# Optimization experiments

Measured on AMD Instinct MI355X. Metric: run time of the kernel, lower is better.

## Reference

```python
import jax, jax.numpy as jnp
import numpy as np

NEG_SLOPE = 0.01  # nn.LeakyReLU default


def setup_inputs() -> dict:
    key = jax.random.key(0)
    ks = jax.random.split(key, 13)
    B, T, C = 128, 2048, 16
    CO = 8 * C          # 128 conv out channels == LSTM input
    H = 128             # LSTM hidden
    G = 4 * H           # gate dim
    OUT = 1
    s = 0.08            # keep recurrence stable over 2048 steps
    f32 = jnp.float32
    return {
        "x": jax.random.normal(ks[0], (B, T, C), f32),
        "conv_w": jax.random.normal(ks[1], (CO, C, 3), f32) * s,
        "conv_b": jax.random.normal(ks[2], (CO,), f32) * s,
        "w_ih0": jax.random.normal(ks[3], (G, CO), f32) * s,
        "w_hh0": jax.random.normal(ks[4], (G, H), f32) * s,
        "b_ih0": jax.random.normal(ks[5], (G,), f32) * s,
        "b_hh0": jax.random.normal(ks[6], (G,), f32) * s,
        "w_ih1": jax.random.normal(ks[7], (G, H), f32) * s,
        "w_hh1": jax.random.normal(ks[8], (G, H), f32) * s,
        "b_ih1": jax.random.normal(ks[9], (G,), f32) * s,
        "b_hh1": jax.random.normal(ks[10], (G,), f32) * s,
        "lin_w": jax.random.normal(ks[11], (OUT, H), f32) * s,
        "lin_b": jax.random.normal(ks[12], (OUT,), f32) * s,
    }


def _lstm_cell(gates, c):
    i, f, g, o = jnp.split(gates, 4, axis=-1)  # torch gate order i,f,g,o
    c_new = jax.nn.sigmoid(f) * c + jax.nn.sigmoid(i) * jnp.tanh(g)
    h_new = jax.nn.sigmoid(o) * jnp.tanh(c_new)
    return h_new, c_new


def reference(x, conv_w, conv_b, w_ih0, w_hh0, b_ih0, b_hh0,
              w_ih1, w_hh1, b_ih1, b_hh1, lin_w, lin_b):
    B, T, C = x.shape
    H = w_hh0.shape[1]
    # Conv1d k=3 pad=1 over time: [B,C,T] -> [B,8C,T]
    xc = jnp.transpose(x, (0, 2, 1))
    y = jax.lax.conv_general_dilated(
        xc, conv_w, window_strides=(1,), padding=((1, 1),),
        dimension_numbers=("NCH", "OIH", "NCH"))
    y = y + conv_b[None, :, None]
    y = jnp.where(y >= 0, y, NEG_SLOPE * y)  # LeakyReLU
    seq = jnp.transpose(y, (0, 2, 1))  # [B,T,8C]
    # Precompute layer-0 input projection (biases folded in, constant per step)
    x0 = jnp.einsum("btc,gc->btg", seq, w_ih0) + (b_ih0 + b_hh0)  # [B,T,4H]
    b1 = b_ih1 + b_hh1

    def step(carry, xt):
        h0, c0, h1, c1 = carry
        h0, c0 = _lstm_cell(xt + h0 @ w_hh0.T, c0)
        h1, c1 = _lstm_cell(h0 @ w_ih1.T + b1 + h1 @ w_hh1.T, c1)
        return (h0, c0, h1, c1), h1

    zeros = jnp.zeros((B, H), x.dtype)
    init = (zeros, zeros, zeros, zeros)
    xs = jnp.transpose(x0, (1, 0, 2))  # [T,B,4H]
    _, hs = jax.lax.scan(step, init, xs)  # [T,B,H]
    pooled = hs.mean(axis=0)  # adaptive_avg_pool1d(.,1) == mean over time
    return pooled @ lin_w.T + lin_b
```

## Files before the change

kernel.cpp:

```cpp
#include <hip/hip_runtime.h>
#include <hip/hip_fp16.h>
#include <cstdint>
#include <cstddef>

#define B_ 128
#define T_ 2048
#define C_ 16
#define CO_ 128
#define H_ 128
#define G_ 512
#define WCV 184
#define NBLK (72 + WCV)
#define L2E  1.4426950408889634f
#define L2E2 2.8853900817779268f

typedef _Float16 half8 __attribute__((ext_vector_type(8)));
typedef float f32x4 __attribute__((ext_vector_type(4)));

__device__ __forceinline__ unsigned packh2f(float a, float b) {
  union { _Float16 h[2]; unsigned u; } x;
  x.h[0] = (_Float16)a; x.h[1] = (_Float16)b;
  return x.u;
}

__device__ __forceinline__ float rcpf(float x) { return __builtin_amdgcn_rcpf(x); }

__device__ __forceinline__ float exp2f_(float x) {
#if __has_builtin(__builtin_amdgcn_exp2f)
  return __builtin_amdgcn_exp2f(x);
#else
  return __expf(x * 0.6931471805599453f);
#endif
}

__device__ __forceinline__ void block_sync() {
  asm volatile("s_waitcnt lgkmcnt(0)" ::: "memory");
  __builtin_amdgcn_s_barrier();
  asm volatile("" ::: "memory");
}

__device__ __forceinline__ int ld_rlx(const int* p) {
  return __hip_atomic_load(p, __ATOMIC_RELAXED, __HIP_MEMORY_SCOPE_AGENT);
}
__device__ __forceinline__ void st_rlx(int* p, int v) {
  __hip_atomic_store(p, v, __ATOMIC_RELAXED, __HIP_MEMORY_SCOPE_AGENT);
}

__device__ __forceinline__ float lstm_cell1(float iv, float fv, float gv,
                                            float ov, float& c) {
  gv = fminf(fmaxf(gv, -43.3f), 43.3f);
  float ei = exp2f_(-iv), ef = exp2f_(-fv), eg = exp2f_(gv);
  float P = (1.f + ei) * (eg + 1.f);
  float Q = 1.f + ef;
  float num = c * P + (eg - 1.f) * Q;
  float cN = num * rcpf(Q * P);
  c = cN;
  float cc = fminf(fmaxf(cN, -15.f), 15.f);
  float eo = exp2f_(-ov), ec = exp2f_(L2E2 * cc);
  return (ec - 1.f) * rcpf((1.f + eo) * (ec + 1.f));
}

__global__ __launch_bounds__(256) void pack_kernel(
    const float* __restrict__ w_ih0, const float* __restrict__ w_hh0,
    const float* __restrict__ w_ih1, const float* __restrict__ w_hh1,
    const float* __restrict__ b_ih1, const float* __restrict__ b_hh1,
    uint4* __restrict__ Wf0, uint4* __restrict__ Wih1f,
    uint4* __restrict__ Whh1f, uint4* __restrict__ WB0f,
    f32x4* __restrict__ b1fD) {
  int tid = blockIdx.x * 256 + threadIdx.x;
  if (tid < 24576) {
    int u = tid & 8191, L = u & 63, s = (u >> 6) & 3, tl = (u >> 8) & 3, w = u >> 10;
    int which = tid >> 13;
    const float* src = (which == 0) ? w_hh0 : (which == 1) ? w_ih1 : w_hh1;
    uint4* dst = (which == 0) ? Wf0 : (which == 1) ? Wih1f : Whh1f;
    int m = (w + 8 * tl) * 16 + (L & 15);
    float sc = (tl == 2) ? L2E2 : L2E;
    int k0 = s * 32 + (L >> 4) * 8;
    const float* p = src + m * 128 + k0;
    uint4 o;
    o.x = packh2f(p[0] * sc, p[1] * sc); o.y = packh2f(p[2] * sc, p[3] * sc);
    o.z = packh2f(p[4] * sc, p[5] * sc); o.w = packh2f(p[6] * sc, p[7] * sc);
    dst[u] = o;
  } else if (tid < 32768) {
    int u = tid - 24576, L = u & 63, s = (u >> 6) & 3, nt = u >> 8;
    int g = nt * 16 + (L & 15);
    float sc = ((nt >> 3) == 2) ? L2E2 : L2E;
    int k0 = s * 32 + (L >> 4) * 8;
    const float* p = w_ih0 + g * 128 + k0;
    uint4 o;
    o.x = packh2f(p[0] * sc, p[1] * sc); o.y = packh2f(p[2] * sc, p[3] * sc);
    o.z = packh2f(p[4] * sc, p[5] * sc); o.w = packh2f(p[6] * sc, p[7] * sc);
    WB0f[u] = o;
  } else if (tid < 34816) {
    int u2 = tid - 32768;
    int tl = u2 & 3, L = (u2 >> 2) & 63, w = u2 >> 8;
    int q = L >> 4;
    float sc = (tl == 2) ? L2E2 : L2E;
    f32x4 o;
#pragma unroll
    for (int reg = 0; reg < 4; ++reg) {
      int row = (w + 8 * tl) * 16 + q * 4 + reg;
      o[reg] = (b_ih1[row] + b_hh1[row]) * sc;
    }
    b1fD[u2] = o;
  }
}

__global__ __launch_bounds__(512, 1) void persist_kernel(
    const float* __restrict__ x, const float* __restrict__ conv_w,
    const float* __restrict__ conv_b, const float* __restrict__ b_ih0,
    const float* __restrict__ b_hh0,
    const uint4* __restrict__ Wf0, const uint4* __restrict__ Wih1f,
    const uint4* __restrict__ Whh1f, const uint4* __restrict__ WB0f,
    const f32x4* __restrict__ b1fD,
    uint4* __restrict__ x0f, uint2* __restrict__ h0g, uint4* __restrict__ z1f,
    float* __restrict__ psave, int* __restrict__ flags,
    int rmask, int rmask2) {
  __shared__ __align__(16) union {
    struct { float xs[34 * 16]; _Float16 yh[32 * 136]; _Float16 x0S[32 * 512]; } wk;
    struct { _Float16 h[2][16 * 136]; float red[8192]; } rc;
  } sm;

  int* xready = flags;
  int* l0p = flags + 2048;
  int* l0c = flags + 2560;
  int* z1p = flags + 3072;
  int* l1p = flags + 3200;

  const int bid = blockIdx.x;
  const int tid = threadIdx.x;
  const int w = tid >> 6, L = tid & 63, q = L >> 4, n = L & 15;

  if (bid < 32 || (bid >= 40 && bid < 72)) {
    const bool isL0 = bid < 32;
    const int rb = isL0 ? bid : bid - 40;
    const int grp = (rb & 7) * 4 + (rb >> 3);
    half8 WA[4][4];
    {
      const uint4* Wsrc = isL0 ? Wf0 : Whh1f;
#pragma unroll
      for (int tl = 0; tl < 4; ++tl)
#pragma unroll
        for (int s = 0; s < 4; ++s)
          WA[tl][s] = __builtin_bit_cast(half8, Wsrc[((w * 4 + tl) * 4 + s) * 64 + L]);
    }
    float cst = 0.f, pool = 0.f;
    for (int idx = tid; idx < 2176; idx += 512) ((unsigned*)sm.rc.h)[idx] = 0u;
    __syncthreads();

    const int n4 = n & 3;
    const int n16 = (grp & 3) * 4 + n4;
    const int uc = w * 16 + (L >> 2);
    const int bc = L & 3;
    const int Lsrc = (L & 0x30) | (L & 3);
    const int rsrc = (L >> 2) & 3;
    float* red = sm.rc.red;

    const uint4* rp = (isL0 ? x0f : z1f) +
        (((size_t)(grp >> 2) * 8 + w) * 64 + (q * 16 + n16)) * 2;
    const int rmk = isL0 ? rmask : rmask2;
    uint2* hgp = h0g + (((grp >> 2) * 16 + ((grp & 3) * 4 + (tid & 3))) * 32 + (tid >> 2));
    uint4 pa[4], pb[4];

    for (int g = 0; g < 64; ++g) {
      const int p0g = g * 32;
      if (tid == 0) {
        if (isL0) {
          while (ld_rlx(&xready[g * 32 + grp]) < 4) __builtin_amdgcn_s_sleep(2);
          if (g < 63)
            while (ld_rlx(&xready[(g + 1) * 32 + grp]) < 4) __builtin_amdgcn_s_sleep(2);
        } else {
          int tgt = p0g + 40; if (tgt > T_) tgt = T_;
          while (ld_rlx(&z1p[(grp >> 2) * 16]) < tgt) __builtin_amdgcn_s_sleep(1);
        }
        __builtin_amdgcn_fence(__ATOMIC_ACQUIRE, "agent");
      }
      block_sync();
      if (g == 0) {
#pragma unroll
        for (int k = 0; k < 4; ++k) {
          pa[k] = rp[(size_t)k * 8192];
          pb[k] = rp[(size_t)k * 8192 + 1];
        }
      }
#pragma unroll 1
      for (int io = 0; io < 8; ++io) {
#pragma unroll
        for (int k = 0; k < 4; ++k) {
          const int t = p0g + io * 4 + k;
          const int c = t & 1, p = c ^ 1;
          f32x4 acc[4];
          {
            half8 xlo = __builtin_bit_cast(half8, pa[k]);
            half8 xhi = __builtin_bit_cast(half8, pb[k]);
            acc[0] = (f32x4){(float)xlo[0], (float)xlo[1], (float)xlo[2], (float)xlo[3]};
            acc[1] = (f32x4){(float)xlo[4], (float)xlo[5], (float)xlo[6], (float)xlo[7]};
            acc[2] = (f32x4){(float)xhi[0], (float)xhi[1], (float)xhi[2], (float)xhi[3]};
            acc[3] = (f32x4){(float)xhi[4], (float)xhi[5], (float)xhi[6], (float)xhi[7]};
          }
          half8 B0[4];
#pragma unroll
          for (int s = 0; s < 4; ++s)
            B0[s] = *(const half8*)&sm.rc.h[p][n4 * 136 + s * 32 + q * 8];
#pragma unroll
          for (int s = 0; s < 4; ++s)
#pragma unroll
            for (int tl = 0; tl < 4; ++tl)
              acc[tl] = __builtin_amdgcn_mfma_f32_16x16x32_f16(WA[tl][s], B0[s], acc[tl], 0, 0, 0);

          {
            int tn = t + 4; if (tn > T_ - 1) tn = T_ - 1;
            const size_t so = (size_t)(tn & rmk) * 8192;
            pa[k] = rp[so];
            pb[k] = rp[so + 1];
          }

#pragma unroll
          for (int tl = 0; tl < 4; ++tl)
            *(f32x4*)&red[((w * 4 + tl) * 64 + L) * 4] = acc[tl];
          asm volatile("s_waitcnt lgkmcnt(0)" ::: "memory");
          float gi = red[((w * 4 + 0) * 64 + Lsrc) * 4 + rsrc];
          float gf = red[((w * 4 + 1) * 64 + Lsrc) * 4 + rsrc];
          float gg = red[((w * 4 + 2) * 64 + Lsrc) * 4 + rsrc];
          float go = red[((w * 4 + 3) * 64 + Lsrc) * 4 + rsrc];
          float hv = lstm_cell1(gi, gf, gg, go, cst);
          if (!isL0) pool += hv;
          sm.rc.h[c][bc * 136 + uc] = (_Float16)hv;

          block_sync();
          if (isL0) {
            if (k == 3) {
              asm volatile("s_waitcnt vmcnt(8)" ::: "memory");
              if (tid == 0) st_rlx(&l0p[grp * 16], t - 3);
            }
            if (tid < 128)
              hgp[(size_t)t * 4096] =
                  *(const uint2*)&sm.rc.h[c][(tid & 3) * 136 + (tid >> 2) * 4];
          }
        }
      }
      if (tid == 0) {
        if (isL0) st_rlx(&l0c[grp * 16], p0g + 32);
        else if (g & 1) st_rlx(&l1p[grp * 16], p0g + 32);
      }
    }
    if (isL0) {
      asm volatile("s_waitcnt vmcnt(0)" ::: "memory");
      __builtin_amdgcn_s_barrier();
      if (tid == 0)
        __hip_atomic_store(&l0p[grp * 16], T_, __ATOMIC_RELEASE,
                           __HIP_MEMORY_SCOPE_AGENT);
    } else {
      psave[(size_t)(grp * 4 + bc) * 128 + uc] = pool;
    }
  } else if (bid < 40) {
    const int b16 = bid - 32;
    half8 WI[4][4];
#pragma unroll
    for (int tl = 0; tl < 4; ++tl)
#pragma unroll
      for (int s = 0; s < 4; ++s)
        WI[tl][s] = __builtin_bit_cast(half8, Wih1f[((w * 4 + tl) * 4 + s) * 64 + L]);
    f32x4 b1v[4];
#pragma unroll
    for (int tl = 0; tl < 4; ++tl) b1v[tl] = b1fD[(w * 64 + L) * 4 + tl];

    const int n2 = tid >> 5, jq = tid & 31;
    const uint2* hsrc = h0g + ((b16 * 16 + n2) * 32 + jq);
    uint4* zdst = z1f + (((size_t)b16 * 8 + w) * 64 + L) * 2;
    const int R2 = rmask2 + 1;
    uint2 hpf[4];

#pragma unroll 1
    for (int p0 = 0; p0 < T_; p0 += 4) {
      if (tid < 4) {
        const int gj = b16 * 4 + tid;
        while (ld_rlx(&l0p[gj * 16]) < p0 + 4) __builtin_amdgcn_s_sleep(1);
        __builtin_amdgcn_fence(__ATOMIC_ACQUIRE, "agent");
      } else if (tid >= 4 && tid < 8 && p0 + 4 > R2) {
        const int gj = b16 * 4 + (tid - 4);
        const int need = p0 + 12 - R2;
        while (ld_rlx(&l1p[gj * 16]) < need) __builtin_amdgcn_s_sleep(8);
      }
      block_sync();
#pragma unroll
      for (int k = 0; k < 4; ++k) hpf[k] = hsrc[(size_t)(p0 + k) * 4096];
#pragma unroll
      for (int k = 0; k < 4; ++k) {
        const int t = p0 + k;
        const int c = t & 1;
        *(uint2*)&sm.rc.h[c][n2 * 136 + jq * 4] = hpf[k];
        block_sync();
        half8 B[4];
#pragma unroll
        for (int s = 0; s < 4; ++s)
          B[s] = *(const half8*)&sm.rc.h[c][n * 136 + s * 32 + q * 8];
        f32x4 acc[4];
#pragma unroll
        for (int tl = 0; tl < 4; ++tl) acc[tl] = b1v[tl];
#pragma unroll
        for (int s = 0; s < 4; ++s)
#pragma unroll
          for (int tl = 0; tl < 4; ++tl)
            acc[tl] = __builtin_amdgcn_mfma_f32_16x16x32_f16(WI[tl][s], B[s], acc[tl], 0, 0, 0);
        uint4 o0, o1;
        o0.x = packh2f(acc[0][0], acc[0][1]); o0.y = packh2f(acc[0][2], acc[0][3]);
        o0.z = packh2f(acc[1][0], acc[1][1]); o0.w = packh2f(acc[1][2], acc[1][3]);
        o1.x = packh2f(acc[2][0], acc[2][1]); o1.y = packh2f(acc[2][2], acc[2][3]);
        o1.z = packh2f(acc[3][0], acc[3][1]); o1.w = packh2f(acc[3][2], acc[3][3]);
        const size_t zs = (size_t)(t & rmask2) * 8192;
        zdst[zs] = o0;
        zdst[zs + 1] = o1;
      }
      asm volatile("s_waitcnt vmcnt(12)" ::: "memory");
      block_sync();
      if (tid == 0) st_rlx(&z1p[b16 * 16], p0);
    }
    asm volatile("s_waitcnt vmcnt(0)" ::: "memory");
    __builtin_amdgcn_s_barrier();
    if (tid == 0)
      __hip_atomic_store(&z1p[b16 * 16], T_, __ATOMIC_RELEASE,
                         __HIP_MEMORY_SCOPE_AGENT);
  } else {
    const int wi = bid - 72;
    const int co = tid & 127;
    float cw[48];
#pragma unroll
    for (int i = 0; i < 12; ++i) {
      const float4 v = *(const float4*)(conv_w + co * 48 + i * 4);
      cw[i * 4 + 0] = v.x; cw[i * 4 + 1] = v.y;
      cw[i * 4 + 2] = v.z; cw[i * 4 + 3] = v.w;
    }
    const float cb = conv_b[co];
    half8 WB[4][4];
#pragma unroll
    for (int nt4 = 0; nt4 < 4; ++nt4)
#pragma unroll
      for (int s = 0; s < 4; ++s)
        WB[nt4][s] = __builtin_bit_cast(half8, WB0f[((w * 4 + nt4) * 4 + s) * 64 + L]);
    float b0v[4];
#pragma unroll
    for (int nt4 = 0; nt4 < 4; ++nt4) {
      int gg = (w * 4 + nt4) * 16 + n;
      b0v[nt4] = (b_ih0[gg] + b_hh0[gg]) * (((gg >> 7) == 2) ? L2E2 : L2E);
    }
    const int R = rmask + 1;

    for (int u = wi; u < 8192; u += WCV) {
      const int tile = u >> 7, b = u & 127;
      const int t0c = tile * 32;
      if (t0c + 40 > R) {
        const int need = t0c + 40 - R;
        if (tid == 0)
          while (ld_rlx(&l0c[(b >> 2) * 16]) < need)
            __builtin_amdgcn_s_sleep(8);
      }
      __syncthreads();

      for (int idx = tid; idx < 544; idx += 512) {
        int row = idx >> 4, cc2 = idx & 15;
        int gt = t0c - 1 + row;
        sm.wk.xs[idx] = (gt >= 0 && gt < T_) ? x[((size_t)b * T_ + gt) * C_ + cc2] : 0.f;
      }
      __syncthreads();

#pragma unroll
      for (int pp = 0; pp < 8; ++pp) {
        int r = pp * 4 + (tid >> 7);
        float acc = cb;
#pragma unroll
        for (int c16 = 0; c16 < 16; ++c16)
#pragma unroll
          for (int kk = 0; kk < 3; ++kk)
            acc += sm.wk.xs[(r + kk) * 16 + c16] * cw[c16 * 3 + kk];
        acc = acc >= 0.f ? acc : 0.01f * acc;
        sm.wk.yh[r * 136 + co] = (_Float16)acc;
      }
      __syncthreads();

#pragma unroll
      for (int mt = 0; mt < 2; ++mt) {
        half8 A[4];
#pragma unroll
        for (int s = 0; s < 4; ++s)
          A[s] = *(const half8*)&sm.wk.yh[(mt * 16 + n) * 136 + s * 32 + q * 8];
#pragma unroll
        for (int nt4 = 0; nt4 < 4; ++nt4) {
          f32x4 acc = {b0v[nt4], b0v[nt4], b0v[nt4], b0v[nt4]};
#pragma unroll
          for (int s = 0; s < 4; ++s)
            acc = __builtin_amdgcn_mfma_f32_16x16x32_f16(A[s], WB[nt4][s], acc, 0, 0, 0);
          int tau = w * 4 + nt4;
          int off = (tau & 7) * 64 + (n >> 2) * 16 + (tau >> 3) * 4 + (n & 3);
#pragma unroll
          for (int reg = 0; reg < 4; ++reg)
            sm.wk.x0S[(mt * 16 + q * 4 + reg) * 512 + off] = (_Float16)acc[reg];
        }
      }
      __syncthreads();

      const int bn = b & 15, bb16 = b >> 4;
      const int trb = t0c & rmask;
#pragma unroll
      for (int kk = 0; kk < 2; ++kk) {
        int cc = kk * 512 + tid;
        int r = cc >> 5, wq = cc & 31;
        int w2 = wq >> 2, q2 = wq & 3;
        const uint4* src = (const uint4*)&sm.wk.x0S[r * 512 + wq * 16];
        size_t gidx = ((((size_t)(trb + r) * 8 + bb16) * 8 + w2) * 64 + (bn + 16 * q2)) * 2;
        x0f[gidx] = src[0];
        x0f[gidx + 1] = src[1];
      }
      asm volatile("s_waitcnt vmcnt(0)" ::: "memory");
      __syncthreads();
      if (tid == 0)
        __hip_atomic_fetch_add(&xready[tile * 32 + (b >> 2)], 1, __ATOMIC_RELEASE,
                               __HIP_MEMORY_SCOPE_AGENT);
    }
  }
}

__global__ __launch_bounds__(128) void final_kernel(
    const float* __restrict__ psave, const float* __restrict__ lin_w,
    const float* __restrict__ lin_b, float* __restrict__ out) {
  int b = threadIdx.x;
  float acc = 0.f;
  const f32x4* pv = (const f32x4*)(psave + (size_t)b * 128);
  const f32x4* lw = (const f32x4*)lin_w;
#pragma unroll
  for (int u = 0; u < 32; ++u) {
    f32x4 v = pv[u], l = lw[u];
    acc += v[0] * l[0] + v[1] * l[1] + v[2] * l[2] + v[3] * l[3];
  }
  out[b] = acc * (1.0f / (float)T_) + lin_b[0];
}

extern "C" void kernel_launch(void* const* d_in, const int* in_sizes, int n_in,
                              void* d_out, int out_size, void* d_ws, size_t ws_size,
                              hipStream_t stream) {
  (void)in_sizes; (void)n_in; (void)out_size;
  const float* x      = (const float*)d_in[0];
  const float* conv_w = (const float*)d_in[1];
  const float* conv_b = (const float*)d_in[2];
  const float* w_ih0  = (const float*)d_in[3];
  const float* w_hh0  = (const float*)d_in[4];
  const float* b_ih0  = (const float*)d_in[5];
  const float* b_hh0  = (const float*)d_in[6];
  const float* w_ih1  = (const float*)d_in[7];
  const float* w_hh1  = (const float*)d_in[8];
  const float* b_ih1  = (const float*)d_in[9];
  const float* b_hh1  = (const float*)d_in[10];
  const float* lin_w  = (const float*)d_in[11];
  const float* lin_b  = (const float*)d_in[12];

  char* ws = (char*)d_ws;
  uint4* Wf0   = (uint4*)(ws + 0);
  uint4* Wih1f = (uint4*)(ws + 131072);
  uint4* Whh1f = (uint4*)(ws + 262144);
  uint4* WB0f  = (uint4*)(ws + 393216);
  f32x4* b1fD  = (f32x4*)(ws + 524288);
  float* psave = (float*)(ws + 557056);
  int*   flags = (int*)(ws + 622592);
  uint2* h0g   = (uint2*)(ws + 638976);
  const size_t base = 638976 + 67108864;

  int R = 256, R2 = 256;
  while (R > 64 && base + ((size_t)R + (size_t)R2) * 131072 > ws_size) {
    R >>= 1; R2 >>= 1;
  }
  uint4* x0f = (uint4*)(ws + base);
  uint4* z1f = (uint4*)(ws + base + (size_t)R * 131072);

  hipMemsetAsync(flags, 0, 16384, stream);
  pack_kernel<<<136, 256, 0, stream>>>(w_ih0, w_hh0, w_ih1, w_hh1, b_ih1, b_hh1,
                                       Wf0, Wih1f, Whh1f, WB0f, b1fD);
  persist_kernel<<<NBLK, 512, 0, stream>>>(
      x, conv_w, conv_b, b_ih0, b_hh0, Wf0, Wih1f, Whh1f, WB0f, b1fD,
      x0f, h0g, z1f, psave, flags, R - 1, R2 - 1);
  final_kernel<<<1, 128, 0, stream>>>(psave, lin_w, lin_b, (float*)d_out);
}
```

Measured before the change: 1.646 ms.

## Fuse layer-1 input projection into layer-0 recurrent blocks, drop h0 round trip

The 8 dedicated blocks that read h0 from global memory and computed the layer-1 input projection are removed. Layer-0 blocks now apply W_ih1 to their previous-step h0 tile, which is already in shared memory, and write z1 straight to the ring buffer. This removes the h0 global buffer, one handoff stage and its flags, and frees 8 blocks for more conv workers. The cost is 16 extra MFMAs per step on the layer-0 critical path, more register pressure, and a new back-pressure wait on layer-1 progress for ring reuse.

```diff
diff --git a/kernel.cpp b/kernel.cpp
--- a/kernel.cpp
+++ b/kernel.cpp
@@ -9,8 +9,8 @@
 #define CO_ 128
 #define H_ 128
 #define G_ 512
-#define WCV 184
-#define NBLK (72 + WCV)
+#define WCV 192
+#define NBLK (64 + WCV)
 #define L2E  1.4426950408889634f
 #define L2E2 2.8853900817779268f
 
@@ -113,7 +113,7 @@
     const uint4* __restrict__ Wf0, const uint4* __restrict__ Wih1f,
     const uint4* __restrict__ Whh1f, const uint4* __restrict__ WB0f,
     const f32x4* __restrict__ b1fD,
-    uint4* __restrict__ x0f, uint2* __restrict__ h0g, uint4* __restrict__ z1f,
+    uint4* __restrict__ x0f, uint4* __restrict__ z1f,
     float* __restrict__ psave, int* __restrict__ flags,
     int rmask, int rmask2) {
   __shared__ __align__(16) union {
@@ -122,18 +122,17 @@
   } sm;
 
   int* xready = flags;
-  int* l0p = flags + 2048;
-  int* l0c = flags + 2560;
-  int* z1p = flags + 3072;
-  int* l1p = flags + 3200;
+  int* l0c = flags + 2048;
+  int* z1p = flags + 2560;
+  int* l1p = flags + 3072;
 
   const int bid = blockIdx.x;
   const int tid = threadIdx.x;
   const int w = tid >> 6, L = tid & 63, q = L >> 4, n = L & 15;
 
-  if (bid < 32 || (bid >= 40 && bid < 72)) {
+  if (bid < 64) {
     const bool isL0 = bid < 32;
-    const int rb = isL0 ? bid : bid - 40;
+    const int rb = isL0 ? bid : bid - 32;
     const int grp = (rb & 7) * 4 + (rb >> 3);
     half8 WA[4][4];
     {
@@ -144,6 +143,20 @@
         for (int s = 0; s < 4; ++s)
           WA[tl][s] = __builtin_bit_cast(half8, Wsrc[((w * 4 + tl) * 4 + s) * 64 + L]);
     }
+    half8 WI[4][4];
+    if (isL0) {
+#pragma unroll
+      for (int tl = 0; tl < 4; ++tl)
+#pragma unroll
+        for (int s = 0; s < 4; ++s)
+          WI[tl][s] = __builtin_bit_cast(half8, Wih1f[((w * 4 + tl) * 4 + s) * 64 + L]);
+    }
+    f32x4 b1v[4];
+    if (!isL0) {
+#pragma unroll
+      for (int tl = 0; tl < 4; ++tl) b1v[tl] = b1fD[(w * 64 + L) * 4 + tl];
+    }
+
     float cst = 0.f, pool = 0.f;
     for (int idx = tid; idx < 2176; idx += 512) ((unsigned*)sm.rc.h)[idx] = 0u;
     __syncthreads();
@@ -156,10 +169,12 @@
     const int rsrc = (L >> 2) & 3;
     float* red = sm.rc.red;
 
+    const int b16 = grp >> 2;
     const uint4* rp = (isL0 ? x0f : z1f) +
-        (((size_t)(grp >> 2) * 8 + w) * 64 + (q * 16 + n16)) * 2;
+        (((size_t)b16 * 8 + w) * 64 + (q * 16 + n16)) * 2;
     const int rmk = isL0 ? rmask : rmask2;
-    uint2* hgp = h0g + (((grp >> 2) * 16 + ((grp & 3) * 4 + (tid & 3))) * 32 + (tid >> 2));
+    uint4* zdst = z1f + (((size_t)b16 * 8 + w) * 64 + (q * 16 + (grp & 3) * 4 + n)) * 2;
+    const int R2 = rmask2 + 1;
     uint4 pa[4], pb[4];
 
     for (int g = 0; g < 64; ++g) {
@@ -169,9 +184,13 @@
           while (ld_rlx(&xready[g * 32 + grp]) < 4) __builtin_amdgcn_s_sleep(2);
           if (g < 63)
             while (ld_rlx(&xready[(g + 1) * 32 + grp]) < 4) __builtin_amdgcn_s_sleep(2);
+          if (p0g + 32 > R2) {
+            const int need = p0g + 40 - R2;
+            while (ld_rlx(&l1p[grp * 16]) < need) __builtin_amdgcn_s_sleep(8);
+          }
         } else {
           int tgt = p0g + 40; if (tgt > T_) tgt = T_;
-          while (ld_rlx(&z1p[(grp >> 2) * 16]) < tgt) __builtin_amdgcn_s_sleep(1);
+          while (ld_rlx(&z1p[grp * 16]) < tgt) __builtin_amdgcn_s_sleep(1);
         }
         __builtin_amdgcn_fence(__ATOMIC_ACQUIRE, "agent");
       }
@@ -189,6 +208,10 @@
         for (int k = 0; k < 4; ++k) {
           const int t = p0g + io * 4 + k;
           const int c = t & 1, p = c ^ 1;
+          half8 B0[4];
+#pragma unroll
+          for (int s = 0; s < 4; ++s)
+            B0[s] = *(const half8*)&sm.rc.h[p][n4 * 136 + s * 32 + q * 8];
           f32x4 acc[4];
           {
             half8 xlo = __builtin_bit_cast(half8, pa[k]);
@@ -197,16 +220,27 @@
             acc[1] = (f32x4){(float)xlo[4], (float)xlo[5], (float)xlo[6], (float)xlo[7]};
             acc[2] = (f32x4){(float)xhi[0], (float)xhi[1], (float)xhi[2], (float)xhi[3]};
             acc[3] = (f32x4){(float)xhi[4], (float)xhi[5], (float)xhi[6], (float)xhi[7]};
+            if (!isL0) {
+              acc[0] += b1v[0]; acc[1] += b1v[1];
+              acc[2] += b1v[2]; acc[3] += b1v[3];
+            }
           }
-          half8 B0[4];
-#pragma unroll
-          for (int s = 0; s < 4; ++s)
-            B0[s] = *(const half8*)&sm.rc.h[p][n4 * 136 + s * 32 + q * 8];
 #pragma unroll
           for (int s = 0; s < 4; ++s)
 #pragma unroll
             for (int tl = 0; tl < 4; ++tl)
               acc[tl] = __builtin_amdgcn_mfma_f32_16x16x32_f16(WA[tl][s], B0[s], acc[tl], 0, 0, 0);
+
+          f32x4 zacc[4];
+          if (isL0) {
+#pragma unroll
+            for (int tl = 0; tl < 4; ++tl) zacc[tl] = (f32x4){0.f, 0.f, 0.f, 0.f};
+#pragma unroll
+            for (int s = 0; s < 4; ++s)
+#pragma unroll
+              for (int tl = 0; tl < 4; ++tl)
+                zacc[tl] = __builtin_amdgcn_mfma_f32_16x16x32_f16(WI[tl][s], B0[s], zacc[tl], 0, 0, 0);
+          }
 
           {
             int tn = t + 4; if (tn > T_ - 1) tn = T_ - 1;
@@ -227,102 +261,63 @@
           if (!isL0) pool += hv;
           sm.rc.h[c][bc * 136 + uc] = (_Float16)hv;
 
+          if (isL0) {
+            uint4 zo0, zo1;
+            zo0.x = packh2f(zacc[0][0], zacc[0][1]); zo0.y = packh2f(zacc[0][2], zacc[0][3]);
+            zo0.z = packh2f(zacc[1][0], zacc[1][1]); zo0.w = packh2f(zacc[1][2], zacc[1][3]);
+            zo1.x = packh2f(zacc[2][0], zacc[2][1]); zo1.y = packh2f(zacc[2][2], zacc[2][3]);
+            zo1.z = packh2f(zacc[3][0], zacc[3][1]); zo1.w = packh2f(zacc[3][2], zacc[3][3]);
+            if (n < 4) {
+              const size_t zs = (size_t)((t - 1) & rmask2) * 8192;
+              zdst[zs] = zo0;
+              zdst[zs + 1] = zo1;
+            }
+            if (k == 3)
+              asm volatile("s_waitcnt vmcnt(12)" ::: "memory");
+          }
           block_sync();
-          if (isL0) {
-            if (k == 3) {
-              asm volatile("s_waitcnt vmcnt(8)" ::: "memory");
-              if (tid == 0) st_rlx(&l0p[grp * 16], t - 3);
-            }
-            if (tid < 128)
-              hgp[(size_t)t * 4096] =
-                  *(const uint2*)&sm.rc.h[c][(tid & 3) * 136 + (tid >> 2) * 4];
-          }
+          if (k == 3 && tid == 0 && isL0)
+            st_rlx(&z1p[grp * 16], t - 3);
         }
       }
       if (tid == 0) {
         if (isL0) st_rlx(&l0c[grp * 16], p0g + 32);
-        else if (g & 1) st_rlx(&l1p[grp * 16], p0g + 32);
+        else st_rlx(&l1p[grp * 16], p0g + 32);
       }
     }
     if (isL0) {
+      half8 B0[4];
+#pragma unroll
+      for (int s = 0; s < 4; ++s)
+        B0[s] = *(const half8*)&sm.rc.h[1][n4 * 136 + s * 32 + q * 8];
+      f32x4 zacc[4];
+#pragma unroll
+      for (int tl = 0; tl < 4; ++tl) zacc[tl] = (f32x4){0.f, 0.f, 0.f, 0.f};
+#pragma unroll
+      for (int s = 0; s < 4; ++s)
+#pragma unroll
+        for (int tl = 0; tl < 4; ++tl)
+          zacc[tl] = __builtin_amdgcn_mfma_f32_16x16x32_f16(WI[tl][s], B0[s], zacc[tl], 0, 0, 0);
+      uint4 zo0, zo1;
+      zo0.x = packh2f(zacc[0][0], zacc[0][1]); zo0.y = packh2f(zacc[0][2], zacc[0][3]);
+      zo0.z = packh2f(zacc[1][0], zacc[1][1]); zo0.w = packh2f(zacc[1][2], zacc[1][3]);
+      zo1.x = packh2f(zacc[2][0], zacc[2][1]); zo1.y = packh2f(zacc[2][2], zacc[2][3]);
+      zo1.z = packh2f(zacc[3][0], zacc[3][1]); zo1.w = packh2f(zacc[3][2], zacc[3][3]);
+      if (n < 4) {
+        const size_t zs = (size_t)((T_ - 1) & rmask2) * 8192;
+        zdst[zs] = zo0;
+        zdst[zs + 1] = zo1;
+      }
       asm volatile("s_waitcnt vmcnt(0)" ::: "memory");
       __builtin_amdgcn_s_barrier();
       if (tid == 0)
-        __hip_atomic_store(&l0p[grp * 16], T_, __ATOMIC_RELEASE,
+        __hip_atomic_store(&z1p[grp * 16], T_, __ATOMIC_RELEASE,
                            __HIP_MEMORY_SCOPE_AGENT);
     } else {
       psave[(size_t)(grp * 4 + bc) * 128 + uc] = pool;
     }
-  } else if (bid < 40) {
-    const int b16 = bid - 32;
-    half8 WI[4][4];
-#pragma unroll
-    for (int tl = 0; tl < 4; ++tl)
-#pragma unroll
-      for (int s = 0; s < 4; ++s)
-        WI[tl][s] = __builtin_bit_cast(half8, Wih1f[((w * 4 + tl) * 4 + s) * 64 + L]);
-    f32x4 b1v[4];
-#pragma unroll
-    for (int tl = 0; tl < 4; ++tl) b1v[tl] = b1fD[(w * 64 + L) * 4 + tl];
-
-    const int n2 = tid >> 5, jq = tid & 31;
-    const uint2* hsrc = h0g + ((b16 * 16 + n2) * 32 + jq);
-    uint4* zdst = z1f + (((size_t)b16 * 8 + w) * 64 + L) * 2;
-    const int R2 = rmask2 + 1;
-    uint2 hpf[4];
-
-#pragma unroll 1
-    for (int p0 = 0; p0 < T_; p0 += 4) {
-      if (tid < 4) {
-        const int gj = b16 * 4 + tid;
-        while (ld_rlx(&l0p[gj * 16]) < p0 + 4) __builtin_amdgcn_s_sleep(1);
-        __builtin_amdgcn_fence(__ATOMIC_ACQUIRE, "agent");
-      } else if (tid >= 4 && tid < 8 && p0 + 4 > R2) {
-        const int gj = b16 * 4 + (tid - 4);
-        const int need = p0 + 12 - R2;
-        while (ld_rlx(&l1p[gj * 16]) < need) __builtin_amdgcn_s_sleep(8);
-      }
-      block_sync();
-#pragma unroll
-      for (int k = 0; k < 4; ++k) hpf[k] = hsrc[(size_t)(p0 + k) * 4096];
-#pragma unroll
-      for (int k = 0; k < 4; ++k) {
-        const int t = p0 + k;
-        const int c = t & 1;
-        *(uint2*)&sm.rc.h[c][n2 * 136 + jq * 4] = hpf[k];
-        block_sync();
-        half8 B[4];
-#pragma unroll
-        for (int s = 0; s < 4; ++s)
-          B[s] = *(const half8*)&sm.rc.h[c][n * 136 + s * 32 + q * 8];
-        f32x4 acc[4];
-#pragma unroll
-        for (int tl = 0; tl < 4; ++tl) acc[tl] = b1v[tl];
-#pragma unroll
-        for (int s = 0; s < 4; ++s)
-#pragma unroll
-          for (int tl = 0; tl < 4; ++tl)
-            acc[tl] = __builtin_amdgcn_mfma_f32_16x16x32_f16(WI[tl][s], B[s], acc[tl], 0, 0, 0);
-        uint4 o0, o1;
-        o0.x = packh2f(acc[0][0], acc[0][1]); o0.y = packh2f(acc[0][2], acc[0][3]);
-        o0.z = packh2f(acc[1][0], acc[1][1]); o0.w = packh2f(acc[1][2], acc[1][3]);
-        o1.x = packh2f(acc[2][0], acc[2][1]); o1.y = packh2f(acc[2][2], acc[2][3]);
-        o1.z = packh2f(acc[3][0], acc[3][1]); o1.w = packh2f(acc[3][2], acc[3][3]);
-        const size_t zs = (size_t)(t & rmask2) * 8192;
-        zdst[zs] = o0;
-        zdst[zs + 1] = o1;
-      }
-      asm volatile("s_waitcnt vmcnt(12)" ::: "memory");
-      block_sync();
-      if (tid == 0) st_rlx(&z1p[b16 * 16], p0);
-    }
-    asm volatile("s_waitcnt vmcnt(0)" ::: "memory");
-    __builtin_amdgcn_s_barrier();
-    if (tid == 0)
-      __hip_atomic_store(&z1p[b16 * 16], T_, __ATOMIC_RELEASE,
-                         __HIP_MEMORY_SCOPE_AGENT);
   } else {
-    const int wi = bid - 72;
+    const int wi = bid - 64;
     const int co = tid & 127;
     float cw[48];
 #pragma unroll
@@ -461,8 +456,7 @@
   f32x4* b1fD  = (f32x4*)(ws + 524288);
   float* psave = (float*)(ws + 557056);
   int*   flags = (int*)(ws + 622592);
-  uint2* h0g   = (uint2*)(ws + 638976);
-  const size_t base = 638976 + 67108864;
+  const size_t base = 622592 + 16384;
 
   int R = 256, R2 = 256;
   while (R > 64 && base + ((size_t)R + (size_t)R2) * 131072 > ws_size) {
@@ -476,6 +470,6 @@
                                        Wf0, Wih1f, Whh1f, WB0f, b1fD);
   persist_kernel<<<NBLK, 512, 0, stream>>>(
       x, conv_w, conv_b, b_ih0, b_hh0, Wf0, Wih1f, Whh1f, WB0f, b1fD,
-      x0f, h0g, z1f, psave, flags, R - 1, R2 - 1);
+      x0f, z1f, psave, flags, R - 1, R2 - 1);
   final_kernel<<<1, 128, 0, stream>>>(psave, lin_w, lin_b, (float*)d_out);
 }
```

Result: slower. 2.021 ms (+22.8%).
